# Kernel optimization log

Measured on AMD Instinct MI355X. Metric: run time of the kernel, lower is better.

## Reference

```python
import jax, jax.numpy as jnp
import numpy as np

NR_AST_NODES = 500_000
NR_CFG_NODES = 100_000
NR_MAPPED = 400_000
AST_DIM = 256
CFG_DIM = 256


def setup_inputs() -> dict:
    key = jax.random.key(0)
    k1, k2, k3, k4, k5 = jax.random.split(key, 5)
    prev = jax.random.normal(k1, (NR_AST_NODES, AST_DIM), dtype=jnp.float32)
    cfg = jax.random.normal(k2, (NR_CFG_NODES, CFG_DIM), dtype=jnp.float32)
    # key indices: unique (a subset permutation) so the scatter is well-defined,
    # mirroring the one-update-per-AST-node mapping in the original data.
    map_key = jax.random.permutation(k3, NR_AST_NODES)[:NR_MAPPED].astype(jnp.int32)
    map_val = jax.random.randint(k4, (NR_MAPPED,), 0, NR_CFG_NODES, dtype=jnp.int32)
    kw1, kw2 = jax.random.split(k5)
    W_update = jax.random.normal(kw1, (CFG_DIM, AST_DIM), dtype=jnp.float32) / np.sqrt(CFG_DIM)
    b_update = jnp.zeros((AST_DIM,), dtype=jnp.float32)
    W_gate = jax.random.normal(kw2, (AST_DIM + AST_DIM, AST_DIM), dtype=jnp.float32) / np.sqrt(2 * AST_DIM)
    b_gate = jnp.zeros((AST_DIM,), dtype=jnp.float32)
    return {
        "previous_ast_nodes_encodings": prev,
        "new_cfg_nodes_encodings": cfg,
        "map_key_indices": map_key,
        "map_val_indices": map_val,
        "W_update": W_update,
        "b_update": b_update,
        "W_gate": W_gate,
        "b_gate": b_gate,
    }


def reference(previous_ast_nodes_encodings, new_cfg_nodes_encodings,
              map_key_indices, map_val_indices,
              W_update, b_update, W_gate, b_gate):
    # gather: previous AST-node states and the macro (CFG) context per mapping entry
    prev_g = previous_ast_nodes_encodings[map_key_indices]        # [M, ast_dim]
    ctx_g = new_cfg_nodes_encodings[map_val_indices]              # [M, cfg_dim]
    # gated StateUpdater (GRU-like gate):
    #   u = tanh(ctx @ W_update + b_update)            -- projected state update
    #   z = sigmoid([prev; u] @ W_gate + b_gate)       -- update gate
    #   new = z * prev + (1 - z) * u
    u = jnp.tanh(ctx_g @ W_update + b_update)                      # [M, ast_dim]
    z = jax.nn.sigmoid(
        prev_g @ W_gate[:AST_DIM] + u @ W_gate[AST_DIM:] + b_gate)  # [M, ast_dim]
    new_states = z * prev_g + (1.0 - z) * u                        # [M, ast_dim]
    # scatter updated rows back into the dense AST-node encodings (dim 0)
    return previous_ast_nodes_encodings.at[map_key_indices].set(new_states)
```

## Files before the change

### kernel.cpp

```cpp
#include <hip/hip_runtime.h>
#include <hip/hip_bf16.h>

#define AST_DIM 256
#define NR_AST 500000
#define NR_CFG 100000
#define NR_MAP 400000

typedef short short8 __attribute__((ext_vector_type(8)));
typedef float f32x4 __attribute__((ext_vector_type(4)));
typedef unsigned long long u64;
typedef unsigned int u32;

__device__ __forceinline__ unsigned short f2bf(float f) {
    u32 u = __float_as_uint(f);
    u += 0x7FFFu + ((u >> 16) & 1u);
    return (unsigned short)(u >> 16);
}
__device__ __forceinline__ float bf2f(unsigned short s) {
    return __uint_as_float(((u32)s) << 16);
}
__device__ __forceinline__ u64 pack4(f32x4 v) {
    __hip_bfloat162 lo = __float22bfloat162_rn(float2{v.x, v.y});
    __hip_bfloat162 hi = __float22bfloat162_rn(float2{v.z, v.w});
    return (u64)(*(u32*)&lo) | ((u64)(*(u32*)&hi) << 32);
}
__device__ __forceinline__ float fast_tanh(float x) {
    return 1.f - 2.f * __builtin_amdgcn_rcpf(__expf(2.f * x) + 1.f);
}
__device__ __forceinline__ float fast_sigmoid(float x) {
    return __builtin_amdgcn_rcpf(1.f + __expf(-x));
}
__device__ __forceinline__ void dma16(const void* g, void* l) {
    __builtin_amdgcn_global_load_lds((const __attribute__((address_space(1))) u32*)g,
                                     (__attribute__((address_space(3))) u32*)l, 16, 0, 0);
}

__global__ void convert_w(const float* __restrict__ Wu, const float* __restrict__ Wg,
                          unsigned short* __restrict__ wt) {
    int idx = blockIdx.x * 256 + threadIdx.x;
    if (idx >= 3 * 65536) return;
    int m = idx >> 16;
    int r = idx & 65535;
    int n = r >> 8;
    int k = r & 255;
    float v;
    if (m == 0)      v = Wu[k * 256 + n];
    else if (m == 1) v = Wg[k * 256 + n];
    else             v = Wg[(k + 256) * 256 + n];
    wt[idx] = f2bf(v);
}

__global__ void set_mask(const int* __restrict__ keys, unsigned char* __restrict__ mask) {
    int i = blockIdx.x * 256 + threadIdx.x;
    if (i < NR_MAP) mask[keys[i]] = 1;
}

__global__ void copy_unmapped(const float* __restrict__ prev,
                              const unsigned char* __restrict__ mask,
                              float* __restrict__ out) {
    const long long total = (long long)NR_AST * 64;
    for (long long i = (long long)blockIdx.x * blockDim.x + threadIdx.x; i < total;
         i += (long long)gridDim.x * blockDim.x) {
        int row = (int)(i >> 6);
        if (!mask[row]) {
            f32x4 v = __builtin_nontemporal_load((const f32x4*)prev + i);
            __builtin_nontemporal_store(v, (f32x4*)out + i);
        }
    }
}

__global__ __launch_bounds__(512, 4) void compute_u(
    const float* __restrict__ cfg, const unsigned short* __restrict__ Wtu,
    const float* __restrict__ bu, unsigned short* __restrict__ u_all) {
    __shared__ __align__(16) unsigned char ctxb[64 * 512];

    const int tid = threadIdx.x;
    const int lane = tid & 63;
    const int wv = tid >> 6;
    const int ln15 = lane & 15;
    const int khi = lane >> 4;
    const int cb = wv * 32;
    const int m0 = blockIdx.x * 64;

#pragma unroll
    for (int i = 0; i < 8; ++i) {
        int r = wv * 8 + i;
        int g = m0 + r;
        if (g >= NR_CFG) g = NR_CFG - 1;
        f32x4 v = *((const f32x4*)(cfg + (size_t)g * AST_DIM) + lane);
        int addr = (r << 9) + ((lane << 3) ^ ((r & 7) << 4));
        *(u64*)(ctxb + addr) = pack4(v);
    }
    __syncthreads();

    const float b0 = bu[cb + ln15], b1 = bu[cb + 16 + ln15];
    f32x4 acc[4][2];
#pragma unroll
    for (int mt = 0; mt < 4; ++mt) {
        acc[mt][0] = f32x4{b0, b0, b0, b0};
        acc[mt][1] = f32x4{b1, b1, b1, b1};
    }
#pragma unroll
    for (int ks = 0; ks < 8; ++ks) {
        short8 a[4], b[2];
#pragma unroll
        for (int mt = 0; mt < 4; ++mt) {
            int row = mt * 16 + ln15;
            int addr = (row << 9) + (((ks << 6) + (khi << 4)) ^ ((row & 7) << 4));
            a[mt] = *(const short8*)(ctxb + addr);
        }
#pragma unroll
        for (int nt = 0; nt < 2; ++nt)
            b[nt] = *(const short8*)(Wtu + (cb + nt * 16 + ln15) * 256 + ks * 32 + khi * 8);
#pragma unroll
        for (int mt = 0; mt < 4; ++mt)
#pragma unroll
            for (int nt = 0; nt < 2; ++nt)
                acc[mt][nt] = __builtin_amdgcn_mfma_f32_16x16x32_bf16(a[mt], b[nt], acc[mt][nt], 0, 0, 0);
    }
#pragma unroll
    for (int mt = 0; mt < 4; ++mt)
#pragma unroll
        for (int rr = 0; rr < 4; ++rr) {
            int row = mt * 16 + khi * 4 + rr;
            int g = m0 + row;
            if (g < NR_CFG) {
#pragma unroll
                for (int nt = 0; nt < 2; ++nt) {
                    int col = cb + nt * 16 + ln15;
                    u_all[(size_t)g * AST_DIM + col] = f2bf(fast_tanh(acc[mt][nt][rr]));
                }
            }
        }
}

__global__ __launch_bounds__(512, 4) void mixer_gate(
    const float* __restrict__ prev, const unsigned short* __restrict__ u_all,
    const int* __restrict__ keys, const int* __restrict__ vals,
    const unsigned short* __restrict__ Wtgt, const unsigned short* __restrict__ Wtgb,
    const float* __restrict__ bg, float* __restrict__ out) {
    __shared__ __align__(16) unsigned char prvb[64 * 512];
    __shared__ __align__(16) unsigned char u_st[64 * 512];

    const int tid = threadIdx.x;
    const int lane = tid & 63;
    const int wv = tid >> 6;
    const int ln15 = lane & 15;
    const int khi = lane >> 4;
    const int cb = wv * 32;
    const int m0 = blockIdx.x * 64;

    const int kv = keys[m0 + lane];
    const int vv = vals[m0 + lane];

#pragma unroll
    for (int i = 0; i < 4; ++i) {
        int r0 = wv * 8 + i * 2;
        int row = r0 + (lane >> 5);
        int vidx = __shfl(vv, row);
        const unsigned short* src = u_all + (size_t)vidx * AST_DIM + (((lane & 31) ^ (row & 7)) << 3);
        dma16(src, u_st + (r0 << 9));
    }
#pragma unroll
    for (int i = 0; i < 8; ++i) {
        int r = wv * 8 + i;
        int kidx = __shfl(kv, r);
        f32x4 v = *((const f32x4*)(prev + (size_t)kidx * AST_DIM) + lane);
        int addr = (r << 9) + ((lane << 3) ^ ((r & 7) << 4));
        *(u64*)(prvb + addr) = pack4(v);
    }
    __syncthreads();

    const float b0 = bg[cb + ln15], b1 = bg[cb + 16 + ln15];
    f32x4 acc[4][2];
#pragma unroll
    for (int mt = 0; mt < 4; ++mt) {
        acc[mt][0] = f32x4{b0, b0, b0, b0};
        acc[mt][1] = f32x4{b1, b1, b1, b1};
    }
#pragma unroll
    for (int ks = 0; ks < 8; ++ks) {
        short8 a[4], b[2];
#pragma unroll
        for (int mt = 0; mt < 4; ++mt) {
            int row = mt * 16 + ln15;
            int addr = (row << 9) + (((ks << 6) + (khi << 4)) ^ ((row & 7) << 4));
            a[mt] = *(const short8*)(prvb + addr);
        }
#pragma unroll
        for (int nt = 0; nt < 2; ++nt)
            b[nt] = *(const short8*)(Wtgt + (cb + nt * 16 + ln15) * 256 + ks * 32 + khi * 8);
#pragma unroll
        for (int mt = 0; mt < 4; ++mt)
#pragma unroll
            for (int nt = 0; nt < 2; ++nt)
                acc[mt][nt] = __builtin_amdgcn_mfma_f32_16x16x32_bf16(a[mt], b[nt], acc[mt][nt], 0, 0, 0);
    }
#pragma unroll
    for (int ks = 0; ks < 8; ++ks) {
        short8 a[4], b[2];
#pragma unroll
        for (int mt = 0; mt < 4; ++mt) {
            int row = mt * 16 + ln15;
            int addr = (row << 9) + ((((ks << 2) + khi) ^ (row & 7)) << 4);
            a[mt] = *(const short8*)(u_st + addr);
        }
#pragma unroll
        for (int nt = 0; nt < 2; ++nt)
            b[nt] = *(const short8*)(Wtgb + (cb + nt * 16 + ln15) * 256 + ks * 32 + khi * 8);
#pragma unroll
        for (int mt = 0; mt < 4; ++mt)
#pragma unroll
            for (int nt = 0; nt < 2; ++nt)
                acc[mt][nt] = __builtin_amdgcn_mfma_f32_16x16x32_bf16(a[mt], b[nt], acc[mt][nt], 0, 0, 0);
    }

#pragma unroll
    for (int mt = 0; mt < 4; ++mt)
#pragma unroll
        for (int rr = 0; rr < 4; ++rr) {
            int row = mt * 16 + khi * 4 + rr;
            int key = __shfl(kv, row);
            float* orow = out + (size_t)key * AST_DIM;
#pragma unroll
            for (int nt = 0; nt < 2; ++nt) {
                int col = cb + nt * 16 + ln15;
                float z = fast_sigmoid(acc[mt][nt][rr]);
                float pf = bf2f(*(const unsigned short*)(prvb + (row << 9) + ((col << 1) ^ ((row & 7) << 4))));
                float uv = bf2f(*(const unsigned short*)(u_st + (row << 9) +
                                ((((col >> 3) ^ (row & 7)) << 4) + ((col & 7) << 1))));
                orow[col] = fmaf(z, pf - uv, uv);
            }
        }
}

__global__ __launch_bounds__(512, 4) void mixer_fused(
    const float* __restrict__ prev, const float* __restrict__ cfg,
    const int* __restrict__ keys, const int* __restrict__ vals,
    const unsigned short* __restrict__ Wtu, const unsigned short* __restrict__ Wtgt,
    const unsigned short* __restrict__ Wtgb, const float* __restrict__ bu,
    const float* __restrict__ bg, float* __restrict__ out) {
    __shared__ __align__(16) unsigned char ctx_lds[64 * 512];
    __shared__ __align__(16) unsigned char prv_lds[64 * 512];

    const int tid = threadIdx.x;
    const int lane = tid & 63;
    const int wave = tid >> 6;
    const int ln15 = lane & 15;
    const int khi = lane >> 4;
    const int cb = wave * 32;
    const int m0 = blockIdx.x * 64;

    const int kv = keys[m0 + lane];
    const int vv = vals[m0 + lane];

#pragma unroll 4
    for (int i = 0; i < 8; ++i) {
        int r = i * 8 + wave;
        f32x4 cv = *((const f32x4*)(cfg + (size_t)__shfl(vv, r) * AST_DIM) + lane);
        f32x4 pv = *((const f32x4*)(prev + (size_t)__shfl(kv, r) * AST_DIM) + lane);
        int addr = (r << 9) + ((lane << 3) ^ ((r & 7) << 4));
        *(u64*)(ctx_lds + addr) = pack4(cv);
        *(u64*)(prv_lds + addr) = pack4(pv);
    }
    __syncthreads();

    f32x4 acc[4][2];
    {
        float b0 = bu[cb + ln15], b1 = bu[cb + 16 + ln15];
        for (int mt = 0; mt < 4; ++mt) {
            acc[mt][0] = f32x4{b0, b0, b0, b0};
            acc[mt][1] = f32x4{b1, b1, b1, b1};
        }
    }
#pragma unroll
    for (int ks = 0; ks < 8; ++ks) {
        short8 a[4], b[2];
        for (int mt = 0; mt < 4; ++mt) {
            int row = mt * 16 + ln15;
            int addr = (row << 9) + (((ks << 6) + (khi << 4)) ^ ((row & 7) << 4));
            a[mt] = *(const short8*)(ctx_lds + addr);
        }
        for (int nt = 0; nt < 2; ++nt)
            b[nt] = *(const short8*)(Wtu + (cb + nt * 16 + ln15) * 256 + ks * 32 + khi * 8);
        for (int mt = 0; mt < 4; ++mt)
            for (int nt = 0; nt < 2; ++nt)
                acc[mt][nt] = __builtin_amdgcn_mfma_f32_16x16x32_bf16(a[mt], b[nt], acc[mt][nt], 0, 0, 0);
    }
    __syncthreads();
#pragma unroll
    for (int mt = 0; mt < 4; ++mt)
        for (int rr = 0; rr < 4; ++rr) {
            int row = mt * 16 + khi * 4 + rr;
            for (int nt = 0; nt < 2; ++nt) {
                int col = cb + nt * 16 + ln15;
                int addr = (row << 9) + ((col << 1) ^ ((row & 7) << 4));
                *(unsigned short*)(ctx_lds + addr) = f2bf(fast_tanh(acc[mt][nt][rr]));
            }
        }
    __syncthreads();
    {
        float b0 = bg[cb + ln15], b1 = bg[cb + 16 + ln15];
        for (int mt = 0; mt < 4; ++mt) {
            acc[mt][0] = f32x4{b0, b0, b0, b0};
            acc[mt][1] = f32x4{b1, b1, b1, b1};
        }
    }
#pragma unroll
    for (int ks = 0; ks < 8; ++ks) {
        short8 a[4], b[2];
        for (int mt = 0; mt < 4; ++mt) {
            int row = mt * 16 + ln15;
            int addr = (row << 9) + (((ks << 6) + (khi << 4)) ^ ((row & 7) << 4));
            a[mt] = *(const short8*)(prv_lds + addr);
        }
        for (int nt = 0; nt < 2; ++nt)
            b[nt] = *(const short8*)(Wtgt + (cb + nt * 16 + ln15) * 256 + ks * 32 + khi * 8);
        for (int mt = 0; mt < 4; ++mt)
            for (int nt = 0; nt < 2; ++nt)
                acc[mt][nt] = __builtin_amdgcn_mfma_f32_16x16x32_bf16(a[mt], b[nt], acc[mt][nt], 0, 0, 0);
    }
#pragma unroll
    for (int ks = 0; ks < 8; ++ks) {
        short8 a[4], b[2];
        for (int mt = 0; mt < 4; ++mt) {
            int row = mt * 16 + ln15;
            int addr = (row << 9) + (((ks << 6) + (khi << 4)) ^ ((row & 7) << 4));
            a[mt] = *(const short8*)(ctx_lds + addr);
        }
        for (int nt = 0; nt < 2; ++nt)
            b[nt] = *(const short8*)(Wtgb + (cb + nt * 16 + ln15) * 256 + ks * 32 + khi * 8);
        for (int mt = 0; mt < 4; ++mt)
            for (int nt = 0; nt < 2; ++nt)
                acc[mt][nt] = __builtin_amdgcn_mfma_f32_16x16x32_bf16(a[mt], b[nt], acc[mt][nt], 0, 0, 0);
    }
#pragma unroll
    for (int mt = 0; mt < 4; ++mt)
        for (int rr = 0; rr < 4; ++rr) {
            int row = mt * 16 + khi * 4 + rr;
            int key = __shfl(kv, row);
            float* orow = out + (size_t)key * AST_DIM;
            for (int nt = 0; nt < 2; ++nt) {
                int col = cb + nt * 16 + ln15;
                int ad = (row << 9) + ((col << 1) ^ ((row & 7) << 4));
                float z = fast_sigmoid(acc[mt][nt][rr]);
                float pf = bf2f(*(const unsigned short*)(prv_lds + ad));
                float uv = bf2f(*(const unsigned short*)(ctx_lds + ad));
                orow[col] = fmaf(z, pf - uv, uv);
            }
        }
}

extern "C" void kernel_launch(void* const* d_in, const int* in_sizes, int n_in,
                              void* d_out, int out_size, void* d_ws, size_t ws_size,
                              hipStream_t stream) {
    const float* prev = (const float*)d_in[0];
    const float* cfg = (const float*)d_in[1];
    const int* keys = (const int*)d_in[2];
    const int* vals = (const int*)d_in[3];
    const float* Wu = (const float*)d_in[4];
    const float* bu = (const float*)d_in[5];
    const float* Wg = (const float*)d_in[6];
    const float* bg = (const float*)d_in[7];
    float* out = (float*)d_out;

    unsigned short* wt = (unsigned short*)d_ws;
    unsigned char* mask = (unsigned char*)d_ws + 3 * 65536 * 2;
    unsigned short* u_all = (unsigned short*)((char*)d_ws + (1 << 20));
    const size_t ws_needed = (size_t)(1 << 20) + (size_t)NR_CFG * AST_DIM * 2;

    (void)hipMemsetAsync(mask, 0, NR_AST, stream);
    convert_w<<<768, 256, 0, stream>>>(Wu, Wg, wt);
    set_mask<<<(NR_MAP + 255) / 256, 256, 0, stream>>>(keys, mask);
    copy_unmapped<<<2048, 256, 0, stream>>>(prev, mask, out);
    if (ws_size >= ws_needed) {
        compute_u<<<(NR_CFG + 63) / 64, 512, 0, stream>>>(cfg, wt, bu, u_all);
        mixer_gate<<<NR_MAP / 64, 512, 0, stream>>>(prev, u_all, keys, vals,
                                                    wt + 65536, wt + 2 * 65536, bg, out);
    } else {
        mixer_fused<<<NR_MAP / 64, 512, 0, stream>>>(prev, cfg, keys, vals, wt, wt + 65536,
                                                     wt + 2 * 65536, bu, bg, out);
    }
}
```

Baseline: 442.7 us.

## Fuse unmapped-row copy into gate kernel via compacted list and smaller tiles

Builds a compacted list of unmapped rows with an atomic counter. The separate copy kernel is replaced by dedicated copy blocks interleaved (one in 13) inside the gate kernel, so the copy traffic overlaps with the MFMA gate work. Gate tiles shrink from 64 to 32 rows to allow higher occupancy, and output stores become nontemporal. The cost is an extra compaction kernel with atomics, less weight reuse per block, and a list that is written in nondeterministic order.

```diff
diff --git a/kernel.cpp b/kernel.cpp
--- a/kernel.cpp
+++ b/kernel.cpp
@@ -5,6 +5,11 @@
 #define NR_AST 500000
 #define NR_CFG 100000
 #define NR_MAP 400000
+#define NR_UNMAP (NR_AST - NR_MAP)
+#define NMIX (NR_MAP / 32)
+#define NTOT 13542
+#define NCOPY 1041
+#define COPY_STRIDE (NCOPY * 8)
 
 typedef short short8 __attribute__((ext_vector_type(8)));
 typedef float f32x4 __attribute__((ext_vector_type(4)));
@@ -55,6 +60,15 @@
     if (i < NR_MAP) mask[keys[i]] = 1;
 }
 
+__global__ void compact_unmapped(const unsigned char* __restrict__ mask,
+                                 int* __restrict__ list, int* __restrict__ counter) {
+    int i = blockIdx.x * 256 + threadIdx.x;
+    if (i < NR_AST && !mask[i]) {
+        int p = atomicAdd(counter, 1);
+        list[p] = i;
+    }
+}
+
 __global__ void copy_unmapped(const float* __restrict__ prev,
                               const unsigned char* __restrict__ mask,
                               float* __restrict__ out) {
@@ -134,36 +148,53 @@
         }
 }
 
-__global__ __launch_bounds__(512, 4) void mixer_gate(
+__global__ __launch_bounds__(512, 8) void fused_main(
     const float* __restrict__ prev, const unsigned short* __restrict__ u_all,
     const int* __restrict__ keys, const int* __restrict__ vals,
+    const int* __restrict__ list,
     const unsigned short* __restrict__ Wtgt, const unsigned short* __restrict__ Wtgb,
     const float* __restrict__ bg, float* __restrict__ out) {
-    __shared__ __align__(16) unsigned char prvb[64 * 512];
-    __shared__ __align__(16) unsigned char u_st[64 * 512];
-
+    __shared__ __align__(16) unsigned char prvb[32 * 512];
+    __shared__ __align__(16) unsigned char u_st[32 * 512];
+
+    const int b = blockIdx.x;
+    const int q = b / 13;
+    const int rmod = b % 13;
     const int tid = threadIdx.x;
     const int lane = tid & 63;
     const int wv = tid >> 6;
+
+    if (rmod == 12) {
+        for (int ci = q * 8 + wv; ci < NR_UNMAP; ci += COPY_STRIDE) {
+            int row = list[ci];
+            f32x4 v = __builtin_nontemporal_load((const f32x4*)(prev + (size_t)row * AST_DIM) + lane);
+            __builtin_nontemporal_store(v, (f32x4*)(out + (size_t)row * AST_DIM) + lane);
+        }
+        return;
+    }
+    const int id = q * 12 + rmod;
+    if (id >= NMIX) return;
+
     const int ln15 = lane & 15;
     const int khi = lane >> 4;
+    const int ln31 = lane & 31;
     const int cb = wv * 32;
-    const int m0 = blockIdx.x * 64;
-
-    const int kv = keys[m0 + lane];
-    const int vv = vals[m0 + lane];
-
-#pragma unroll
-    for (int i = 0; i < 4; ++i) {
-        int r0 = wv * 8 + i * 2;
+    const int m0 = id * 32;
+
+    const int kv = keys[m0 + ln31];
+    const int vv = vals[m0 + ln31];
+
+#pragma unroll
+    for (int i = 0; i < 2; ++i) {
+        int r0 = wv * 4 + i * 2;
         int row = r0 + (lane >> 5);
         int vidx = __shfl(vv, row);
-        const unsigned short* src = u_all + (size_t)vidx * AST_DIM + (((lane & 31) ^ (row & 7)) << 3);
+        const unsigned short* src = u_all + (size_t)vidx * AST_DIM + ((ln31 ^ (row & 7)) << 3);
         dma16(src, u_st + (r0 << 9));
     }
 #pragma unroll
-    for (int i = 0; i < 8; ++i) {
-        int r = wv * 8 + i;
+    for (int i = 0; i < 4; ++i) {
+        int r = wv * 4 + i;
         int kidx = __shfl(kv, r);
         f32x4 v = *((const f32x4*)(prev + (size_t)kidx * AST_DIM) + lane);
         int addr = (r << 9) + ((lane << 3) ^ ((r & 7) << 4));
@@ -172,51 +203,50 @@
     __syncthreads();
 
     const float b0 = bg[cb + ln15], b1 = bg[cb + 16 + ln15];
-    f32x4 acc[4][2];
-#pragma unroll
-    for (int mt = 0; mt < 4; ++mt) {
-        acc[mt][0] = f32x4{b0, b0, b0, b0};
-        acc[mt][1] = f32x4{b1, b1, b1, b1};
-    }
-#pragma unroll
-    for (int ks = 0; ks < 8; ++ks) {
-        short8 a[4], b[2];
-#pragma unroll
-        for (int mt = 0; mt < 4; ++mt) {
+    f32x4 acc[2][2];
+    acc[0][0] = f32x4{b0, b0, b0, b0};
+    acc[0][1] = f32x4{b1, b1, b1, b1};
+    acc[1][0] = acc[0][0];
+    acc[1][1] = acc[0][1];
+#pragma unroll
+    for (int ks = 0; ks < 8; ++ks) {
+        short8 a[2], bfr[2];
+#pragma unroll
+        for (int mt = 0; mt < 2; ++mt) {
             int row = mt * 16 + ln15;
             int addr = (row << 9) + (((ks << 6) + (khi << 4)) ^ ((row & 7) << 4));
             a[mt] = *(const short8*)(prvb + addr);
         }
 #pragma unroll
         for (int nt = 0; nt < 2; ++nt)
-            b[nt] = *(const short8*)(Wtgt + (cb + nt * 16 + ln15) * 256 + ks * 32 + khi * 8);
-#pragma unroll
-        for (int mt = 0; mt < 4; ++mt)
-#pragma unroll
-            for (int nt = 0; nt < 2; ++nt)
-                acc[mt][nt] = __builtin_amdgcn_mfma_f32_16x16x32_bf16(a[mt], b[nt], acc[mt][nt], 0, 0, 0);
-    }
-#pragma unroll
-    for (int ks = 0; ks < 8; ++ks) {
-        short8 a[4], b[2];
-#pragma unroll
-        for (int mt = 0; mt < 4; ++mt) {
+            bfr[nt] = *(const short8*)(Wtgt + (cb + nt * 16 + ln15) * 256 + ks * 32 + khi * 8);
+#pragma unroll
+        for (int mt = 0; mt < 2; ++mt)
+#pragma unroll
+            for (int nt = 0; nt < 2; ++nt)
+                acc[mt][nt] = __builtin_amdgcn_mfma_f32_16x16x32_bf16(a[mt], bfr[nt], acc[mt][nt], 0, 0, 0);
+    }
+#pragma unroll
+    for (int ks = 0; ks < 8; ++ks) {
+        short8 a[2], bfr[2];
+#pragma unroll
+        for (int mt = 0; mt < 2; ++mt) {
             int row = mt * 16 + ln15;
             int addr = (row << 9) + ((((ks << 2) + khi) ^ (row & 7)) << 4);
             a[mt] = *(const short8*)(u_st + addr);
         }
 #pragma unroll
         for (int nt = 0; nt < 2; ++nt)
-            b[nt] = *(const short8*)(Wtgb + (cb + nt * 16 + ln15) * 256 + ks * 32 + khi * 8);
-#pragma unroll
-        for (int mt = 0; mt < 4; ++mt)
-#pragma unroll
-            for (int nt = 0; nt < 2; ++nt)
-                acc[mt][nt] = __builtin_amdgcn_mfma_f32_16x16x32_bf16(a[mt], b[nt], acc[mt][nt], 0, 0, 0);
-    }
-
-#pragma unroll
-    for (int mt = 0; mt < 4; ++mt)
+            bfr[nt] = *(const short8*)(Wtgb + (cb + nt * 16 + ln15) * 256 + ks * 32 + khi * 8);
+#pragma unroll
+        for (int mt = 0; mt < 2; ++mt)
+#pragma unroll
+            for (int nt = 0; nt < 2; ++nt)
+                acc[mt][nt] = __builtin_amdgcn_mfma_f32_16x16x32_bf16(a[mt], bfr[nt], acc[mt][nt], 0, 0, 0);
+    }
+
+#pragma unroll
+    for (int mt = 0; mt < 2; ++mt)
 #pragma unroll
         for (int rr = 0; rr < 4; ++rr) {
             int row = mt * 16 + khi * 4 + rr;
@@ -229,7 +259,7 @@
                 float pf = bf2f(*(const unsigned short*)(prvb + (row << 9) + ((col << 1) ^ ((row & 7) << 4))));
                 float uv = bf2f(*(const unsigned short*)(u_st + (row << 9) +
                                 ((((col >> 3) ^ (row & 7)) << 4) + ((col & 7) << 1))));
-                orow[col] = fmaf(z, pf - uv, uv);
+                __builtin_nontemporal_store(fmaf(z, pf - uv, uv), orow + col);
             }
         }
 }
@@ -366,18 +396,21 @@
 
     unsigned short* wt = (unsigned short*)d_ws;
     unsigned char* mask = (unsigned char*)d_ws + 3 * 65536 * 2;
-    unsigned short* u_all = (unsigned short*)((char*)d_ws + (1 << 20));
-    const size_t ws_needed = (size_t)(1 << 20) + (size_t)NR_CFG * AST_DIM * 2;
-
-    (void)hipMemsetAsync(mask, 0, NR_AST, stream);
+    int* counter = (int*)((char*)d_ws + 917504);
+    int* list = (int*)((char*)d_ws + 983040);
+    unsigned short* u_all = (unsigned short*)((char*)d_ws + (2u << 20));
+    const size_t ws_needed = (size_t)(2u << 20) + (size_t)NR_CFG * AST_DIM * 2;
+
+    (void)hipMemsetAsync(mask, 0, 917504 + 4 - 3 * 65536 * 2, stream);
     convert_w<<<768, 256, 0, stream>>>(Wu, Wg, wt);
     set_mask<<<(NR_MAP + 255) / 256, 256, 0, stream>>>(keys, mask);
-    copy_unmapped<<<2048, 256, 0, stream>>>(prev, mask, out);
     if (ws_size >= ws_needed) {
+        compact_unmapped<<<(NR_AST + 255) / 256, 256, 0, stream>>>(mask, list, counter);
         compute_u<<<(NR_CFG + 63) / 64, 512, 0, stream>>>(cfg, wt, bu, u_all);
-        mixer_gate<<<NR_MAP / 64, 512, 0, stream>>>(prev, u_all, keys, vals,
-                                                    wt + 65536, wt + 2 * 65536, bg, out);
+        fused_main<<<NTOT, 512, 0, stream>>>(prev, u_all, keys, vals, list,
+                                             wt + 65536, wt + 2 * 65536, bg, out);
     } else {
+        copy_unmapped<<<2048, 256, 0, stream>>>(prev, mask, out);
         mixer_fused<<<NR_MAP / 64, 512, 0, stream>>>(prev, cfg, keys, vals, wt, wt + 65536,
                                                      wt + 2 * 65536, bu, bg, out);
     }
```

Result: slower. 680.1 us (+53.6%).

## Stream all AST rows in key order with inverse map, fusing copy and gate

Applied to the files above, without the earlier changes.

Replaces the mask-based copy pass and the key-ordered scatter kernel with one kernel that walks every AST row in order. An inverse map (AST row to CFG index, -1 if unmapped) is built first. Each block reads prev contiguously, copies unmapped rows straight to the output, and computes the gate only for mapped rows, writing results sequentially. This removes the random gather/scatter on prev and out plus the separate copy pass. In exchange, blocks with unmapped rows still run the full MFMA work on those rows, and a 2 MB memset is added.

```diff
diff --git a/kernel.cpp b/kernel.cpp
--- a/kernel.cpp
+++ b/kernel.cpp
@@ -5,6 +5,7 @@
 #define NR_AST 500000
 #define NR_CFG 100000
 #define NR_MAP 400000
+#define NBLK_MAIN ((NR_AST + 63) / 64)
 
 typedef short short8 __attribute__((ext_vector_type(8)));
 typedef float f32x4 __attribute__((ext_vector_type(4)));
@@ -50,6 +51,186 @@
     wt[idx] = f2bf(v);
 }
 
+__global__ void build_vor(const int* __restrict__ keys, const int* __restrict__ vals,
+                          int* __restrict__ vor) {
+    int i = blockIdx.x * 256 + threadIdx.x;
+    if (i < NR_MAP) vor[keys[i]] = vals[i];
+}
+
+__global__ __launch_bounds__(512, 4) void compute_u(
+    const float* __restrict__ cfg, const unsigned short* __restrict__ Wtu,
+    const float* __restrict__ bu, unsigned short* __restrict__ u_all) {
+    __shared__ __align__(16) unsigned char ctxb[64 * 512];
+
+    const int tid = threadIdx.x;
+    const int lane = tid & 63;
+    const int wv = tid >> 6;
+    const int ln15 = lane & 15;
+    const int khi = lane >> 4;
+    const int cb = wv * 32;
+    const int m0 = blockIdx.x * 64;
+
+#pragma unroll
+    for (int i = 0; i < 8; ++i) {
+        int r = wv * 8 + i;
+        int g = m0 + r;
+        if (g >= NR_CFG) g = NR_CFG - 1;
+        f32x4 v = *((const f32x4*)(cfg + (size_t)g * AST_DIM) + lane);
+        int addr = (r << 9) + ((lane << 3) ^ ((r & 7) << 4));
+        *(u64*)(ctxb + addr) = pack4(v);
+    }
+    __syncthreads();
+
+    const float b0 = bu[cb + ln15], b1 = bu[cb + 16 + ln15];
+    f32x4 acc[4][2];
+#pragma unroll
+    for (int mt = 0; mt < 4; ++mt) {
+        acc[mt][0] = f32x4{b0, b0, b0, b0};
+        acc[mt][1] = f32x4{b1, b1, b1, b1};
+    }
+#pragma unroll
+    for (int ks = 0; ks < 8; ++ks) {
+        short8 a[4], b[2];
+#pragma unroll
+        for (int mt = 0; mt < 4; ++mt) {
+            int row = mt * 16 + ln15;
+            int addr = (row << 9) + (((ks << 6) + (khi << 4)) ^ ((row & 7) << 4));
+            a[mt] = *(const short8*)(ctxb + addr);
+        }
+#pragma unroll
+        for (int nt = 0; nt < 2; ++nt)
+            b[nt] = *(const short8*)(Wtu + (cb + nt * 16 + ln15) * 256 + ks * 32 + khi * 8);
+#pragma unroll
+        for (int mt = 0; mt < 4; ++mt)
+#pragma unroll
+            for (int nt = 0; nt < 2; ++nt)
+                acc[mt][nt] = __builtin_amdgcn_mfma_f32_16x16x32_bf16(a[mt], b[nt], acc[mt][nt], 0, 0, 0);
+    }
+#pragma unroll
+    for (int mt = 0; mt < 4; ++mt)
+#pragma unroll
+        for (int rr = 0; rr < 4; ++rr) {
+            int row = mt * 16 + khi * 4 + rr;
+            int g = m0 + row;
+            if (g < NR_CFG) {
+#pragma unroll
+                for (int nt = 0; nt < 2; ++nt) {
+                    int col = cb + nt * 16 + ln15;
+                    u_all[(size_t)g * AST_DIM + col] = f2bf(fast_tanh(acc[mt][nt][rr]));
+                }
+            }
+        }
+}
+
+__global__ __launch_bounds__(512, 4) void stream_main(
+    const float* __restrict__ prev, const unsigned short* __restrict__ u_all,
+    const int* __restrict__ vor,
+    const unsigned short* __restrict__ Wtgt, const unsigned short* __restrict__ Wtgb,
+    const float* __restrict__ bg, float* __restrict__ out) {
+    __shared__ __align__(16) unsigned char prvb[64 * 512];
+    __shared__ __align__(16) unsigned char u_st[64 * 512];
+
+    const int tid = threadIdx.x;
+    const int lane = tid & 63;
+    const int wv = tid >> 6;
+    const int ln15 = lane & 15;
+    const int khi = lane >> 4;
+    const int ln31 = lane & 31;
+    const int cb = wv * 32;
+    const int m0 = blockIdx.x * 64;
+
+    int vr = -1;
+    if (m0 + lane < NR_AST) vr = vor[m0 + lane];
+
+#pragma unroll
+    for (int i = 0; i < 4; ++i) {
+        int r0 = wv * 8 + i * 2;
+        int row = r0 + (lane >> 5);
+        int vidx = __shfl(vr, row);
+        int vsrc = vidx < 0 ? 0 : vidx;
+        const unsigned short* src = u_all + (size_t)vsrc * AST_DIM + ((ln31 ^ (row & 7)) << 3);
+        dma16(src, u_st + (r0 << 9));
+    }
+#pragma unroll
+    for (int i = 0; i < 8; ++i) {
+        int r = wv * 8 + i;
+        int g = m0 + r;
+        if (g < NR_AST) {
+            f32x4 v = __builtin_nontemporal_load((const f32x4*)(prev + (size_t)g * AST_DIM) + lane);
+            int addr = (r << 9) + ((lane << 3) ^ ((r & 7) << 4));
+            *(u64*)(prvb + addr) = pack4(v);
+            if (__shfl(vr, r) < 0)
+                __builtin_nontemporal_store(v, (f32x4*)(out + (size_t)g * AST_DIM) + lane);
+        }
+    }
+    __syncthreads();
+
+    const float b0 = bg[cb + ln15], b1 = bg[cb + 16 + ln15];
+    f32x4 acc[4][2];
+#pragma unroll
+    for (int mt = 0; mt < 4; ++mt) {
+        acc[mt][0] = f32x4{b0, b0, b0, b0};
+        acc[mt][1] = f32x4{b1, b1, b1, b1};
+    }
+#pragma unroll
+    for (int ks = 0; ks < 8; ++ks) {
+        short8 a[4], bfr[2];
+#pragma unroll
+        for (int mt = 0; mt < 4; ++mt) {
+            int row = mt * 16 + ln15;
+            int addr = (row << 9) + (((ks << 6) + (khi << 4)) ^ ((row & 7) << 4));
+            a[mt] = *(const short8*)(prvb + addr);
+        }
+#pragma unroll
+        for (int nt = 0; nt < 2; ++nt)
+            bfr[nt] = *(const short8*)(Wtgt + (cb + nt * 16 + ln15) * 256 + ks * 32 + khi * 8);
+#pragma unroll
+        for (int mt = 0; mt < 4; ++mt)
+#pragma unroll
+            for (int nt = 0; nt < 2; ++nt)
+                acc[mt][nt] = __builtin_amdgcn_mfma_f32_16x16x32_bf16(a[mt], bfr[nt], acc[mt][nt], 0, 0, 0);
+    }
+#pragma unroll
+    for (int ks = 0; ks < 8; ++ks) {
+        short8 a[4], bfr[2];
+#pragma unroll
+        for (int mt = 0; mt < 4; ++mt) {
+            int row = mt * 16 + ln15;
+            int addr = (row << 9) + ((((ks << 2) + khi) ^ (row & 7)) << 4);
+            a[mt] = *(const short8*)(u_st + addr);
+        }
+#pragma unroll
+        for (int nt = 0; nt < 2; ++nt)
+            bfr[nt] = *(const short8*)(Wtgb + (cb + nt * 16 + ln15) * 256 + ks * 32 + khi * 8);
+#pragma unroll
+        for (int mt = 0; mt < 4; ++mt)
+#pragma unroll
+            for (int nt = 0; nt < 2; ++nt)
+                acc[mt][nt] = __builtin_amdgcn_mfma_f32_16x16x32_bf16(a[mt], bfr[nt], acc[mt][nt], 0, 0, 0);
+    }
+
+#pragma unroll
+    for (int mt = 0; mt < 4; ++mt)
+#pragma unroll
+        for (int rr = 0; rr < 4; ++rr) {
+            int row = mt * 16 + khi * 4 + rr;
+            int g = m0 + row;
+            int vrow = __shfl(vr, row);
+            if (g < NR_AST && vrow >= 0) {
+                float* orow = out + (size_t)g * AST_DIM;
+#pragma unroll
+                for (int nt = 0; nt < 2; ++nt) {
+                    int col = cb + nt * 16 + ln15;
+                    float z = fast_sigmoid(acc[mt][nt][rr]);
+                    float pf = bf2f(*(const unsigned short*)(prvb + (row << 9) + ((col << 1) ^ ((row & 7) << 4))));
+                    float uv = bf2f(*(const unsigned short*)(u_st + (row << 9) +
+                                    ((((col >> 3) ^ (row & 7)) << 4) + ((col & 7) << 1))));
+                    __builtin_nontemporal_store(fmaf(z, pf - uv, uv), orow + col);
+                }
+            }
+        }
+}
+
 __global__ void set_mask(const int* __restrict__ keys, unsigned char* __restrict__ mask) {
     int i = blockIdx.x * 256 + threadIdx.x;
     if (i < NR_MAP) mask[keys[i]] = 1;
@@ -67,171 +248,6 @@
             __builtin_nontemporal_store(v, (f32x4*)out + i);
         }
     }
-}
-
-__global__ __launch_bounds__(512, 4) void compute_u(
-    const float* __restrict__ cfg, const unsigned short* __restrict__ Wtu,
-    const float* __restrict__ bu, unsigned short* __restrict__ u_all) {
-    __shared__ __align__(16) unsigned char ctxb[64 * 512];
-
-    const int tid = threadIdx.x;
-    const int lane = tid & 63;
-    const int wv = tid >> 6;
-    const int ln15 = lane & 15;
-    const int khi = lane >> 4;
-    const int cb = wv * 32;
-    const int m0 = blockIdx.x * 64;
-
-#pragma unroll
-    for (int i = 0; i < 8; ++i) {
-        int r = wv * 8 + i;
-        int g = m0 + r;
-        if (g >= NR_CFG) g = NR_CFG - 1;
-        f32x4 v = *((const f32x4*)(cfg + (size_t)g * AST_DIM) + lane);
-        int addr = (r << 9) + ((lane << 3) ^ ((r & 7) << 4));
-        *(u64*)(ctxb + addr) = pack4(v);
-    }
-    __syncthreads();
-
-    const float b0 = bu[cb + ln15], b1 = bu[cb + 16 + ln15];
-    f32x4 acc[4][2];
-#pragma unroll
-    for (int mt = 0; mt < 4; ++mt) {
-        acc[mt][0] = f32x4{b0, b0, b0, b0};
-        acc[mt][1] = f32x4{b1, b1, b1, b1};
-    }
-#pragma unroll
-    for (int ks = 0; ks < 8; ++ks) {
-        short8 a[4], b[2];
-#pragma unroll
-        for (int mt = 0; mt < 4; ++mt) {
-            int row = mt * 16 + ln15;
-            int addr = (row << 9) + (((ks << 6) + (khi << 4)) ^ ((row & 7) << 4));
-            a[mt] = *(const short8*)(ctxb + addr);
-        }
-#pragma unroll
-        for (int nt = 0; nt < 2; ++nt)
-            b[nt] = *(const short8*)(Wtu + (cb + nt * 16 + ln15) * 256 + ks * 32 + khi * 8);
-#pragma unroll
-        for (int mt = 0; mt < 4; ++mt)
-#pragma unroll
-            for (int nt = 0; nt < 2; ++nt)
-                acc[mt][nt] = __builtin_amdgcn_mfma_f32_16x16x32_bf16(a[mt], b[nt], acc[mt][nt], 0, 0, 0);
-    }
-#pragma unroll
-    for (int mt = 0; mt < 4; ++mt)
-#pragma unroll
-        for (int rr = 0; rr < 4; ++rr) {
-            int row = mt * 16 + khi * 4 + rr;
-            int g = m0 + row;
-            if (g < NR_CFG) {
-#pragma unroll
-                for (int nt = 0; nt < 2; ++nt) {
-                    int col = cb + nt * 16 + ln15;
-                    u_all[(size_t)g * AST_DIM + col] = f2bf(fast_tanh(acc[mt][nt][rr]));
-                }
-            }
-        }
-}
-
-__global__ __launch_bounds__(512, 4) void mixer_gate(
-    const float* __restrict__ prev, const unsigned short* __restrict__ u_all,
-    const int* __restrict__ keys, const int* __restrict__ vals,
-    const unsigned short* __restrict__ Wtgt, const unsigned short* __restrict__ Wtgb,
-    const float* __restrict__ bg, float* __restrict__ out) {
-    __shared__ __align__(16) unsigned char prvb[64 * 512];
-    __shared__ __align__(16) unsigned char u_st[64 * 512];
-
-    const int tid = threadIdx.x;
-    const int lane = tid & 63;
-    const int wv = tid >> 6;
-    const int ln15 = lane & 15;
-    const int khi = lane >> 4;
-    const int cb = wv * 32;
-    const int m0 = blockIdx.x * 64;
-
-    const int kv = keys[m0 + lane];
-    const int vv = vals[m0 + lane];
-
-#pragma unroll
-    for (int i = 0; i < 4; ++i) {
-        int r0 = wv * 8 + i * 2;
-        int row = r0 + (lane >> 5);
-        int vidx = __shfl(vv, row);
-        const unsigned short* src = u_all + (size_t)vidx * AST_DIM + (((lane & 31) ^ (row & 7)) << 3);
-        dma16(src, u_st + (r0 << 9));
-    }
-#pragma unroll
-    for (int i = 0; i < 8; ++i) {
-        int r = wv * 8 + i;
-        int kidx = __shfl(kv, r);
-        f32x4 v = *((const f32x4*)(prev + (size_t)kidx * AST_DIM) + lane);
-        int addr = (r << 9) + ((lane << 3) ^ ((r & 7) << 4));
-        *(u64*)(prvb + addr) = pack4(v);
-    }
-    __syncthreads();
-
-    const float b0 = bg[cb + ln15], b1 = bg[cb + 16 + ln15];
-    f32x4 acc[4][2];
-#pragma unroll
-    for (int mt = 0; mt < 4; ++mt) {
-        acc[mt][0] = f32x4{b0, b0, b0, b0};
-        acc[mt][1] = f32x4{b1, b1, b1, b1};
-    }
-#pragma unroll
-    for (int ks = 0; ks < 8; ++ks) {
-        short8 a[4], b[2];
-#pragma unroll
-        for (int mt = 0; mt < 4; ++mt) {
-            int row = mt * 16 + ln15;
-            int addr = (row << 9) + (((ks << 6) + (khi << 4)) ^ ((row & 7) << 4));
-            a[mt] = *(const short8*)(prvb + addr);
-        }
-#pragma unroll
-        for (int nt = 0; nt < 2; ++nt)
-            b[nt] = *(const short8*)(Wtgt + (cb + nt * 16 + ln15) * 256 + ks * 32 + khi * 8);
-#pragma unroll
-        for (int mt = 0; mt < 4; ++mt)
-#pragma unroll
-            for (int nt = 0; nt < 2; ++nt)
-                acc[mt][nt] = __builtin_amdgcn_mfma_f32_16x16x32_bf16(a[mt], b[nt], acc[mt][nt], 0, 0, 0);
-    }
-#pragma unroll
-    for (int ks = 0; ks < 8; ++ks) {
-        short8 a[4], b[2];
-#pragma unroll
-        for (int mt = 0; mt < 4; ++mt) {
-            int row = mt * 16 + ln15;
-            int addr = (row << 9) + ((((ks << 2) + khi) ^ (row & 7)) << 4);
-            a[mt] = *(const short8*)(u_st + addr);
-        }
-#pragma unroll
-        for (int nt = 0; nt < 2; ++nt)
-            b[nt] = *(const short8*)(Wtgb + (cb + nt * 16 + ln15) * 256 + ks * 32 + khi * 8);
-#pragma unroll
-        for (int mt = 0; mt < 4; ++mt)
-#pragma unroll
-            for (int nt = 0; nt < 2; ++nt)
-                acc[mt][nt] = __builtin_amdgcn_mfma_f32_16x16x32_bf16(a[mt], b[nt], acc[mt][nt], 0, 0, 0);
-    }
-
-#pragma unroll
-    for (int mt = 0; mt < 4; ++mt)
-#pragma unroll
-        for (int rr = 0; rr < 4; ++rr) {
-            int row = mt * 16 + khi * 4 + rr;
-            int key = __shfl(kv, row);
-            float* orow = out + (size_t)key * AST_DIM;
-#pragma unroll
-            for (int nt = 0; nt < 2; ++nt) {
-                int col = cb + nt * 16 + ln15;
-                float z = fast_sigmoid(acc[mt][nt][rr]);
-                float pf = bf2f(*(const unsigned short*)(prvb + (row << 9) + ((col << 1) ^ ((row & 7) << 4))));
-                float uv = bf2f(*(const unsigned short*)(u_st + (row << 9) +
-                                ((((col >> 3) ^ (row & 7)) << 4) + ((col & 7) << 1))));
-                orow[col] = fmaf(z, pf - uv, uv);
-            }
-        }
 }
 
 __global__ __launch_bounds__(512, 4) void mixer_fused(
@@ -365,19 +381,22 @@
     float* out = (float*)d_out;
 
     unsigned short* wt = (unsigned short*)d_ws;
-    unsigned char* mask = (unsigned char*)d_ws + 3 * 65536 * 2;
-    unsigned short* u_all = (unsigned short*)((char*)d_ws + (1 << 20));
-    const size_t ws_needed = (size_t)(1 << 20) + (size_t)NR_CFG * AST_DIM * 2;
-
-    (void)hipMemsetAsync(mask, 0, NR_AST, stream);
+    int* vor = (int*)((char*)d_ws + (1u << 20));
+    unsigned short* u_all = (unsigned short*)((char*)d_ws + (4u << 20));
+    const size_t ws_needed = (size_t)(4u << 20) + (size_t)NR_CFG * AST_DIM * 2;
+
     convert_w<<<768, 256, 0, stream>>>(Wu, Wg, wt);
-    set_mask<<<(NR_MAP + 255) / 256, 256, 0, stream>>>(keys, mask);
-    copy_unmapped<<<2048, 256, 0, stream>>>(prev, mask, out);
     if (ws_size >= ws_needed) {
+        (void)hipMemsetAsync(vor, 0xFF, (size_t)NR_AST * 4, stream);
+        build_vor<<<(NR_MAP + 255) / 256, 256, 0, stream>>>(keys, vals, vor);
         compute_u<<<(NR_CFG + 63) / 64, 512, 0, stream>>>(cfg, wt, bu, u_all);
-        mixer_gate<<<NR_MAP / 64, 512, 0, stream>>>(prev, u_all, keys, vals,
-                                                    wt + 65536, wt + 2 * 65536, bg, out);
+        stream_main<<<NBLK_MAIN, 512, 0, stream>>>(prev, u_all, vor,
+                                                   wt + 65536, wt + 2 * 65536, bg, out);
     } else {
+        unsigned char* mask = (unsigned char*)d_ws + 3 * 65536 * 2;
+        (void)hipMemsetAsync(mask, 0, NR_AST, stream);
+        set_mask<<<(NR_MAP + 255) / 256, 256, 0, stream>>>(keys, mask);
+        copy_unmapped<<<2048, 256, 0, stream>>>(prev, mask, out);
         mixer_fused<<<NR_MAP / 64, 512, 0, stream>>>(prev, cfg, keys, vals, wt, wt + 65536,
                                                      wt + 2 * 65536, bu, bg, out);
     }
```

Result: slower. 455.7 us (+3.0%).
